# Kernel optimization log

Measured on AMD Instinct MI355X. Metric: run time of the kernel, lower is better.

Reference implementation:

```python
import jax, jax.numpy as jnp
import numpy as np

D_MODEL = 1024
N_HEADS = 16
POINT_DIM = 4
PLUCKER_DIM = 6
PAIRS4 = [(0, 1), (0, 2), (0, 3), (1, 2), (1, 3), (2, 3)]
_J6 = jnp.array([[0, 0, 0, 0, 0, 1], [0, 0, 0, 0, -1, 0], [0, 0, 0, 1, 0, 0],
                 [0, 0, 1, 0, 0, 0], [0, -1, 0, 0, 0, 0], [1, 0, 0, 0, 0, 0]], dtype=jnp.float32)


def exterior(p1, p2):
    # p1, p2: [..., point_dim] -> normalized Plucker coords [..., 6]
    L = jnp.stack([p1[..., i] * p2[..., j] - p1[..., j] * p2[..., i] for i, j in PAIRS4], axis=-1)
    n = jnp.linalg.norm(L, axis=-1, keepdims=True)
    return L / jnp.maximum(n, 1e-12)


def setup_inputs() -> dict:
    key = jax.random.key(0)
    ks = jax.random.split(key, 16)
    B, T, D, H, pd = 2, 1024, D_MODEL, N_HEADS, POINT_DIM
    s = 0.02
    return {
        "x": jax.random.normal(ks[0], (B, T, D), dtype=jnp.float32),
        "qkv_w": jax.random.normal(ks[1], (D, 3 * D), dtype=jnp.float32) * s,
        "qkv_b": jnp.zeros((3 * D,), dtype=jnp.float32),
        "w1_write_w": jax.random.normal(ks[2], (2 * D, pd * H), dtype=jnp.float32) * s,
        "w2_write_w": jax.random.normal(ks[3], (D, pd * H), dtype=jnp.float32) * s,
        "w1_read_w": jax.random.normal(ks[4], (D, pd * H), dtype=jnp.float32) * s,
        "w2_read_w": jax.random.normal(ks[5], (D, pd * H), dtype=jnp.float32) * s,
        "mem_value_w": jax.random.normal(ks[6], (D, D), dtype=jnp.float32) * s,
        "mem_value_b": jnp.zeros((D,), dtype=jnp.float32),
        "mem_gate_w": jax.random.normal(ks[7], (D, H), dtype=jnp.float32) * s,
        "mem_gate_b": jnp.zeros((H,), dtype=jnp.float32),
        "mem_scale": jnp.full((H,), 0.1, dtype=jnp.float32),
        "out_w": jax.random.normal(ks[8], (D, D), dtype=jnp.float32) * s,
        "out_b": jnp.zeros((D,), dtype=jnp.float32),
        "decay_logits": jnp.full((H,), 4.6, dtype=jnp.float32),
        "J": _J6,
    }


def reference(x, qkv_w, qkv_b, w1_write_w, w2_write_w, w1_read_w, w2_read_w,
              mem_value_w, mem_value_b, mem_gate_w, mem_gate_b, mem_scale,
              out_w, out_b, decay_logits, J):
    B, T, D = x.shape
    H = N_HEADS
    dh = D // H
    pd = POINT_DIM
    scale = dh ** (-0.5)

    # ---- standard causal attention ----
    qkv = (x @ qkv_w + qkv_b).reshape(B, T, 3, H, dh)
    q = jnp.transpose(qkv[:, :, 0], (0, 2, 1, 3))  # [B,H,T,dh]
    k = jnp.transpose(qkv[:, :, 1], (0, 2, 1, 3))
    v = jnp.transpose(qkv[:, :, 2], (0, 2, 1, 3))
    scores = jnp.einsum('bhtd,bhsd->bhts', q, k) * scale
    causal_mask = jnp.triu(jnp.ones((T, T), dtype=bool), k=1)
    scores = jnp.where(causal_mask, -jnp.inf, scores)
    attn = jax.nn.softmax(scores, axis=-1)
    seq_out = jnp.einsum('bhts,bhsd->bthd', attn, v).reshape(B, T, D)

    # ---- trigram write lines ----
    z = jnp.zeros((B, 1, D), dtype=x.dtype)
    x_prev1 = jnp.concatenate([z, x[:, :-1]], axis=1)
    x_prev2 = jnp.concatenate([z, z, x[:, :-2]], axis=1)
    trigram_ctx = jnp.concatenate([x_prev2, x_prev1], axis=-1)  # [B,T,2D]
    w1 = (trigram_ctx @ w1_write_w).reshape(B, T, H, pd)
    w2 = (x @ w2_write_w).reshape(B, T, H, pd)
    write_lines = exterior(w1, w2)  # [B,T,H,6]
    r1 = (x @ w1_read_w).reshape(B, T, H, pd)
    r2 = (x @ w2_read_w).reshape(B, T, H, pd)
    read_lines = exterior(r1, r2)  # [B,T,H,6]

    # ---- Plucker incidence + decay weighting ----
    J_write = jnp.einsum('bshi,ij->bshj', write_lines, J)
    incidence = jnp.einsum('bthi,bshi->bhts', read_lines, J_write)  # [B,H,T,T]
    incidence_sq = incidence ** 2
    positions = jnp.arange(T, dtype=x.dtype)
    diffs = positions[:, None] - positions[None, :]  # [T,T]
    decays = jax.nn.sigmoid(decay_logits)  # [H]
    # strictly-causal (diffs>0) decay weights; masked_fill(triu diag=0, 0) == (diffs>0)
    weights = jnp.where(diffs[None] > 0, decays[:, None, None] ** jnp.maximum(diffs, 0.0)[None], 0.0)
    mem_score = jnp.sum(incidence_sq * weights[None], axis=-1)  # [B,H,T]

    # ---- gated memory value ----
    mem_val = x @ mem_value_w + mem_value_b  # [B,T,D]
    gate = jax.nn.sigmoid(x @ mem_gate_w + mem_gate_b)  # [B,T,H]
    mem_score_t = jnp.transpose(mem_score, (0, 2, 1))  # [B,T,H]
    gated = jax.nn.sigmoid(mem_score_t * mem_scale[None, None, :]) * gate
    gated = jnp.mean(gated, axis=-1, keepdims=True)  # [B,T,1]

    return (seq_out + gated * mem_val) @ out_w + out_b
```

## Files before the change

kernel.cpp:

```cpp
#include <hip/hip_runtime.h>
#include <hip/hip_bf16.h>
#include <stdint.h>


typedef __attribute__((ext_vector_type(8))) __bf16 bf16v8;
typedef __attribute__((ext_vector_type(8))) short  s16x8;
typedef __attribute__((ext_vector_type(4))) float  f32x4;

#define LOG2E 1.4426950408889634f

__device__ __forceinline__ float bf2f(short s) {
  union { uint32_t u; float f; } cv; cv.u = ((uint32_t)(uint16_t)s) << 16; return cv.f;
}
__device__ __forceinline__ short f2bf(float f) {
  union { float f; uint32_t u; } cv; cv.f = f;
  uint32_t r = cv.u + 0x7fffu + ((cv.u >> 16) & 1u);
  return (short)(r >> 16);
}

__device__ __forceinline__ f32x4 mfma_bf16(s16x8 a, s16x8 b, f32x4 c) {
  return __builtin_amdgcn_mfma_f32_16x16x32_bf16(
      __builtin_bit_cast(bf16v8, a), __builtin_bit_cast(bf16v8, b), c, 0, 0, 0);
}

__device__ __forceinline__ void gload_lds16(const void* g, void* l) {
  __builtin_amdgcn_global_load_lds(
      (const __attribute__((address_space(1))) uint32_t*)g,
      (__attribute__((address_space(3))) uint32_t*)l, 16, 0, 0);
}


__global__ __launch_bounds__(256) void k_prep(
    const float* __restrict__ x, const float* __restrict__ qkvw,
    const float* __restrict__ mvw, const float* __restrict__ ow,
    const float* __restrict__ w1w, const float* __restrict__ w2w,
    const float* __restrict__ r1w, const float* __restrict__ r2w,
    const float* __restrict__ gw, const float* __restrict__ qkvb,
    const float* __restrict__ mvb,
    short* __restrict__ xb, short* __restrict__ btall, short* __restrict__ owT,
    float* __restrict__ biasAll) {
  __shared__ float tile[32][33];
  const int bid = blockIdx.x;
  const int tid = threadIdx.x;
  if (bid < 2048) {
    const int i = (bid * 256 + tid) * 4;
    float4 v = *(const float4*)&x[i];
    short4 o;
    o.x = f2bf(v.x); o.y = f2bf(v.y); o.z = f2bf(v.z); o.w = f2bf(v.w);
    *(short4*)&xb[i] = o;
    return;
  }
  if (bid < 7168) {
    const float* W; short* Wt; int N, u;
    if (bid < 5120)      { W = qkvw; Wt = btall;                       N = 3072; u = bid - 2048; }
    else if (bid < 6144) { W = mvw;  Wt = btall + (size_t)3072 * 1024; N = 1024; u = bid - 5120; }
    else                 { W = ow;   Wt = owT;                         N = 1024; u = bid - 6144; }
    const int ntiles = N >> 5;
    const int n0 = (u % ntiles) * 32, k0 = (u / ntiles) * 32;
    const int tx = tid & 31, ty = tid >> 5;
#pragma unroll
    for (int i = 0; i < 4; i++)
      tile[ty + i * 8][tx] = W[(size_t)(k0 + ty + i * 8) * N + n0 + tx];
    __syncthreads();
#pragma unroll
    for (int i = 0; i < 4; i++)
      Wt[(size_t)(n0 + ty + i * 8) * 1024 + k0 + tx] = f2bf(tile[tx][ty + i * 8]);
    return;
  }
  if (bid < 8704) {
    const int idx = (bid - 7168) * 256 + tid;
    const int r = idx >> 10, k = idx & 1023;
    float v = 0.f;
    if (r < 64)       v = w1w[(size_t)k * 64 + r];
    else if (r < 128) v = w1w[(size_t)(1024 + k) * 64 + (r - 64)];
    else if (r < 192) v = w2w[(size_t)k * 64 + (r - 128)];
    else if (r < 256) v = r1w[(size_t)k * 64 + (r - 192)];
    else if (r < 320) v = r2w[(size_t)k * 64 + (r - 256)];
    else if (r < 336) v = gw[(size_t)k * 16 + (r - 320)];
    btall[(size_t)4096 * 1024 + idx] = f2bf(v);
    return;
  }
  {
    const int i = (bid - 8704) * 256 + tid;
    if (i < 4480) {
      float v = 0.f;
      if (i < 3072) v = qkvb[i];
      else if (i < 4096) v = mvb[i - 3072];
      biasAll[i] = v;
    }
  }
}


__global__ __launch_bounds__(256) void k_gemmF(const short* __restrict__ A,
                                               const short* __restrict__ Bt,
                                               short* __restrict__ C,
                                               const float* __restrict__ bias,
                                               float* __restrict__ projf) {
  const int N = 4480, K = 1024;
  __shared__ short As[2][128 * 32];
  __shared__ short Bs[2][128 * 32];
  const int m0 = blockIdx.x * 128, n0 = blockIdx.y * 128;
  const int tid = threadIdx.x;
  const int lane = tid & 63, w = tid >> 6;
  const int wr = (w >> 1) * 64, wc = (w & 1) * 64;
  const int l15 = lane & 15, lg = lane >> 4;
  const int r0e = tid >> 2, c0e = (tid & 3) << 3;
  const int r1e = (tid + 256) >> 2, c1e = ((tid + 256) & 3) << 3;
  f32x4 acc[4][4] = {};

  gload_lds16(A + (size_t)(m0 + r0e) * K + c0e, &As[0][tid * 8]);
  gload_lds16(A + (size_t)(m0 + r1e) * K + c1e, &As[0][(tid + 256) * 8]);
  gload_lds16(Bt + (size_t)(n0 + r0e) * K + c0e, &Bs[0][tid * 8]);
  gload_lds16(Bt + (size_t)(n0 + r1e) * K + c1e, &Bs[0][(tid + 256) * 8]);
  __syncthreads();

  const int nkt = K >> 5;
  for (int kt = 0; kt < nkt; kt++) {
    const int cur = kt & 1;
    if (kt + 1 < nkt) {
      const int k0n = (kt + 1) << 5;
      const int nxt = cur ^ 1;
      gload_lds16(A + (size_t)(m0 + r0e) * K + k0n + c0e, &As[nxt][tid * 8]);
      gload_lds16(A + (size_t)(m0 + r1e) * K + k0n + c1e, &As[nxt][(tid + 256) * 8]);
      gload_lds16(Bt + (size_t)(n0 + r0e) * K + k0n + c0e, &Bs[nxt][tid * 8]);
      gload_lds16(Bt + (size_t)(n0 + r1e) * K + k0n + c1e, &Bs[nxt][(tid + 256) * 8]);
    }
    s16x8 af[4], bfv[4];
#pragma unroll
    for (int i = 0; i < 4; i++) {
      af[i]  = *(const s16x8*)&As[cur][(wr + i * 16 + l15) * 32 + lg * 8];
      bfv[i] = *(const s16x8*)&Bs[cur][(wc + i * 16 + l15) * 32 + lg * 8];
    }
    __builtin_amdgcn_s_setprio(1);
#pragma unroll
    for (int mi = 0; mi < 4; mi++)
#pragma unroll
      for (int ni = 0; ni < 4; ni++)
        acc[mi][ni] = mfma_bf16(af[mi], bfv[ni], acc[mi][ni]);
    __builtin_amdgcn_s_setprio(0);
    __syncthreads();
  }
  const bool isproj = (n0 >= 4096);
#pragma unroll
  for (int mi = 0; mi < 4; mi++)
#pragma unroll
    for (int ni = 0; ni < 4; ni++) {
      const int col = n0 + wc + ni * 16 + l15;
      const float bv = bias[col];
#pragma unroll
      for (int r = 0; r < 4; r++) {
        const int row = m0 + wr + mi * 16 + lg * 4 + r;
        const float v = acc[mi][ni][r] + bv;
        if (isproj) projf[(size_t)row * 384 + (col - 4096)] = v;
        else        C[(size_t)row * 4480 + col] = f2bf(v);
      }
    }
}


template <int BM>
__global__ __launch_bounds__(256) void k_gemm(const short* __restrict__ A,
                                              const short* __restrict__ Bt,
                                              float* __restrict__ C,
                                              const float* __restrict__ bias,
                                              int N, int K) {
  constexpr int MI = BM / 32;
  __shared__ short As[2][BM * 32];
  __shared__ short Bs[2][128 * 32];
  const int m0 = blockIdx.x * BM, n0 = blockIdx.y * 128;
  const int tid = threadIdx.x;
  const int lane = tid & 63, w = tid >> 6;
  const int wr = (w >> 1) * (BM / 2), wc = (w & 1) * 64;
  const int l15 = lane & 15, lg = lane >> 4;
  const int r0e = tid >> 2, c0e = (tid & 3) << 3;
  const int r1e = (tid + 256) >> 2, c1e = ((tid + 256) & 3) << 3;
  f32x4 acc[MI][4] = {};

  auto stage = [&](int buf, int k0) {
    if constexpr (BM == 128) {
      gload_lds16(A + (size_t)(m0 + r0e) * K + k0 + c0e, &As[buf][tid * 8]);
      gload_lds16(A + (size_t)(m0 + r1e) * K + k0 + c1e, &As[buf][(tid + 256) * 8]);
    } else {
      gload_lds16(A + (size_t)(m0 + r0e) * K + k0 + c0e, &As[buf][tid * 8]);
    }
    gload_lds16(Bt + (size_t)(n0 + r0e) * K + k0 + c0e, &Bs[buf][tid * 8]);
    gload_lds16(Bt + (size_t)(n0 + r1e) * K + k0 + c1e, &Bs[buf][(tid + 256) * 8]);
  };

  stage(0, 0);
  __syncthreads();
  const int nkt = K >> 5;
  for (int kt = 0; kt < nkt; kt++) {
    const int cur = kt & 1;
    if (kt + 1 < nkt) stage(cur ^ 1, (kt + 1) << 5);
    s16x8 af[MI], bfv[4];
#pragma unroll
    for (int i = 0; i < MI; i++)
      af[i] = *(const s16x8*)&As[cur][(wr + i * 16 + l15) * 32 + lg * 8];
#pragma unroll
    for (int i = 0; i < 4; i++)
      bfv[i] = *(const s16x8*)&Bs[cur][(wc + i * 16 + l15) * 32 + lg * 8];
    __builtin_amdgcn_s_setprio(1);
#pragma unroll
    for (int mi = 0; mi < MI; mi++)
#pragma unroll
      for (int ni = 0; ni < 4; ni++)
        acc[mi][ni] = mfma_bf16(af[mi], bfv[ni], acc[mi][ni]);
    __builtin_amdgcn_s_setprio(0);
    __syncthreads();
  }
#pragma unroll
  for (int mi = 0; mi < MI; mi++)
#pragma unroll
    for (int ni = 0; ni < 4; ni++) {
      const int col = n0 + wc + ni * 16 + l15;
      const float bv = bias ? bias[col] : 0.f;
#pragma unroll
      for (int r = 0; r < 4; r++) {
        const int row = m0 + wr + mi * 16 + lg * 4 + r;
        C[(size_t)row * N + col] = acc[mi][ni][r] + bv;
      }
    }
}


__global__ void k_vtr(const short* __restrict__ fused, short* __restrict__ vtg) {
  __shared__ short tile[32][33];
  const int bh = blockIdx.z;
  const int b = bh >> 4, h = bh & 15;
  const int t0 = blockIdx.x * 32, d0 = blockIdx.y * 32;
  const int tx = threadIdx.x, ty = threadIdx.y;
#pragma unroll
  for (int i = 0; i < 4; i++)
    tile[ty + i * 8][tx] =
        fused[(size_t)(b * 1024 + t0 + ty + i * 8) * 4480 + 2048 + h * 64 + d0 + tx];
  __syncthreads();
#pragma unroll
  for (int i = 0; i < 4; i++)
    vtg[(size_t)(bh * 64 + d0 + ty + i * 8) * 1024 + t0 + tx] = tile[tx][ty + i * 8];
}


__global__ __launch_bounds__(256) void k_attn(const short* __restrict__ fused,
                                              const short* __restrict__ vtg,
                                              float* __restrict__ Of,
                                              float* __restrict__ Ml) {
  const int id = blockIdx.x;
  const int j = 15 - (id >> 6);
  const int rem = id & 63;
  const int sid = rem >> 5, bh = rem & 31;
  const int b = bh >> 4, h = bh & 15;
  const int tid = threadIdx.x, lane = tid & 63, w = tid >> 6;
  const int l15 = lane & 15, lg = lane >> 4;
  const int q0 = j * 64;
  const int nkv = j + 1;
  const int half = (nkv + 1) >> 1;
  const int lo = sid ? half : 0;
  const int hi = sid ? nkv : half;
  const int pidx = ((j * 32 + bh) << 1) | sid;

  __shared__ short Kl[64 * 72];
  __shared__ short Vt[64 * 72];
  __shared__ short Pl[4][16 * 72];
  const short* base = fused + (size_t)b * 1024 * 4480;
  const short* vbase = vtg + (size_t)bh * 64 * 1024;

  const int e0 = tid, e1 = tid + 256;
  const int r0e = e0 >> 3, c0e = (e0 & 7) << 3;
  const int r1e = e1 >> 3, c1e = (e1 & 7) << 3;

  s16x8 qf[2];
#pragma unroll
  for (int ks = 0; ks < 2; ks++)
    qf[ks] = *(const s16x8*)&base[(size_t)(q0 + w * 16 + l15) * 4480 +
                                  h * 64 + ks * 32 + lg * 8];

  f32x4 O[4] = {};
  float m_run[4], l_run[4];
#pragma unroll
  for (int r = 0; r < 4; r++) { m_run[r] = -1e30f; l_run[r] = 0.f; }

  if (lo < hi) {
    const int kv0 = lo * 64;
    s16x8 ka = *(const s16x8*)&base[(size_t)(kv0 + r0e) * 4480 + 1024 + h * 64 + c0e];
    s16x8 kb = *(const s16x8*)&base[(size_t)(kv0 + r1e) * 4480 + 1024 + h * 64 + c1e];
    s16x8 va = *(const s16x8*)&vbase[(size_t)r0e * 1024 + kv0 + c0e];
    s16x8 vb = *(const s16x8*)&vbase[(size_t)r1e * 1024 + kv0 + c1e];
    *(s16x8*)&Kl[r0e * 72 + c0e] = ka;
    *(s16x8*)&Kl[r1e * 72 + c1e] = kb;
    *(s16x8*)&Vt[r0e * 72 + c0e] = va;
    *(s16x8*)&Vt[r1e * 72 + c1e] = vb;
  }
  __syncthreads();

  for (int kt = lo; kt < hi; kt++) {
    const int kv0 = kt * 64;
    const bool pf = (kt + 1 < hi);
    s16x8 kn0, kn1, vn0, vn1;
    if (pf) {
      const int kvn = kv0 + 64;
      kn0 = *(const s16x8*)&base[(size_t)(kvn + r0e) * 4480 + 1024 + h * 64 + c0e];
      kn1 = *(const s16x8*)&base[(size_t)(kvn + r1e) * 4480 + 1024 + h * 64 + c1e];
      vn0 = *(const s16x8*)&vbase[(size_t)r0e * 1024 + kvn + c0e];
      vn1 = *(const s16x8*)&vbase[(size_t)r1e * 1024 + kvn + c1e];
    }

    f32x4 S[4] = {};
    __builtin_amdgcn_s_setprio(1);
#pragma unroll
    for (int sf = 0; sf < 4; sf++) {
      s16x8 kf0 = *(const s16x8*)&Kl[(sf * 16 + l15) * 72 + lg * 8];
      s16x8 kf1 = *(const s16x8*)&Kl[(sf * 16 + l15) * 72 + 32 + lg * 8];
      S[sf] = mfma_bf16(qf[0], kf0, S[sf]);
      S[sf] = mfma_bf16(qf[1], kf1, S[sf]);
    }
    __builtin_amdgcn_s_setprio(0);

    const bool diag = (kt == j);
    float sv[4][4];
#pragma unroll
    for (int sf = 0; sf < 4; sf++)
#pragma unroll
      for (int r = 0; r < 4; r++) {
        float vv = S[sf][r] * 0.125f;
        if (diag) {
          const int sg = kv0 + sf * 16 + l15;
          const int qg = q0 + w * 16 + lg * 4 + r;
          if (sg > qg) vv = -1e30f;
        }
        sv[sf][r] = vv;
      }
#pragma unroll
    for (int r = 0; r < 4; r++) {
      float pm = fmaxf(fmaxf(sv[0][r], sv[1][r]), fmaxf(sv[2][r], sv[3][r]));
      pm = fmaxf(pm, __shfl_xor(pm, 1, 64));
      pm = fmaxf(pm, __shfl_xor(pm, 2, 64));
      pm = fmaxf(pm, __shfl_xor(pm, 4, 64));
      pm = fmaxf(pm, __shfl_xor(pm, 8, 64));
      if (pm > m_run[r] + 8.f) {
        const float fac = exp2f((m_run[r] - pm) * LOG2E);
        m_run[r] = pm;
        l_run[r] *= fac;
#pragma unroll
        for (int nf = 0; nf < 4; nf++) O[nf][r] *= fac;
      }
      float rs = 0.f;
#pragma unroll
      for (int sf = 0; sf < 4; sf++) {
        float p = (sv[sf][r] <= -1e29f) ? 0.f : exp2f((sv[sf][r] - m_run[r]) * LOG2E);
        rs += p;
        Pl[w][(lg * 4 + r) * 72 + sf * 16 + l15] = f2bf(p);
      }
      rs += __shfl_xor(rs, 1, 64);
      rs += __shfl_xor(rs, 2, 64);
      rs += __shfl_xor(rs, 4, 64);
      rs += __shfl_xor(rs, 8, 64);
      l_run[r] += rs;
    }

    __builtin_amdgcn_s_setprio(1);
#pragma unroll
    for (int ks = 0; ks < 2; ks++) {
      s16x8 pfr = *(const s16x8*)&Pl[w][l15 * 72 + ks * 32 + lg * 8];
#pragma unroll
      for (int nf = 0; nf < 4; nf++) {
        s16x8 vf = *(const s16x8*)&Vt[(nf * 16 + l15) * 72 + ks * 32 + lg * 8];
        O[nf] = mfma_bf16(pfr, vf, O[nf]);
      }
    }
    __builtin_amdgcn_s_setprio(0);

    __syncthreads();
    if (pf) {
      *(s16x8*)&Kl[r0e * 72 + c0e] = kn0;
      *(s16x8*)&Kl[r1e * 72 + c1e] = kn1;
      *(s16x8*)&Vt[r0e * 72 + c0e] = vn0;
      *(s16x8*)&Vt[r1e * 72 + c1e] = vn1;
      __syncthreads();
    }
  }

  float* ob = Of + (size_t)pidx * 4096;
  float* mb = Ml + (size_t)pidx * 128;
#pragma unroll
  for (int r = 0; r < 4; r++) {
    const int rloc = w * 16 + lg * 4 + r;
#pragma unroll
    for (int nf = 0; nf < 4; nf++)
      ob[rloc * 64 + nf * 16 + l15] = O[nf][r];
    if (l15 == 0) {
      mb[rloc] = m_run[r];
      mb[64 + rloc] = l_run[r];
    }
  }
}


__device__ __forceinline__ void exterior6(const float p1[4], const float p2[4], float L[6]) {
  L[0] = p1[0] * p2[1] - p1[1] * p2[0];
  L[1] = p1[0] * p2[2] - p1[2] * p2[0];
  L[2] = p1[0] * p2[3] - p1[3] * p2[0];
  L[3] = p1[1] * p2[2] - p1[2] * p2[1];
  L[4] = p1[1] * p2[3] - p1[3] * p2[1];
  L[5] = p1[2] * p2[3] - p1[3] * p2[2];
  float n = sqrtf(L[0] * L[0] + L[1] * L[1] + L[2] * L[2] +
                  L[3] * L[3] + L[4] * L[4] + L[5] * L[5]);
  float inv = 1.f / fmaxf(n, 1e-12f);
#pragma unroll
  for (int j = 0; j < 6; j++) L[j] *= inv;
}

__global__ void k_lines(const float* __restrict__ proj, const float* __restrict__ Jm,
                        float* __restrict__ jw, float* __restrict__ rl) {
  const int idx = blockIdx.x * 256 + threadIdx.x;
  const int t = idx & 1023, h = (idx >> 10) & 15, b = idx >> 14;
  const int n = b * 1024 + t;
  const int bh = b * 16 + h;
  float p1[4], p2[4], L[6];
#pragma unroll
  for (int p = 0; p < 4; p++) {
    float a  = (t >= 2) ? proj[(size_t)(n - 2) * 384 + h * 4 + p] : 0.f;
    float bb = (t >= 1) ? proj[(size_t)(n - 1) * 384 + 64 + h * 4 + p] : 0.f;
    p1[p] = a + bb;
    p2[p] = proj[(size_t)n * 384 + 128 + h * 4 + p];
  }
  exterior6(p1, p2, L);
  const size_t jo = (size_t)bh * 6144 + t;
#pragma unroll
  for (int j = 0; j < 6; j++) {
    float s = 0.f;
#pragma unroll
    for (int i = 0; i < 6; i++) s += L[i] * Jm[i * 6 + j];
    jw[jo + (size_t)j * 1024] = s;
  }
#pragma unroll
  for (int p = 0; p < 4; p++) {
    p1[p] = proj[(size_t)n * 384 + 192 + h * 4 + p];
    p2[p] = proj[(size_t)n * 384 + 256 + h * 4 + p];
  }
  exterior6(p1, p2, L);
  const size_t ro = ((size_t)bh * 1024 + t) * 6;
#pragma unroll
  for (int j = 0; j < 6; j++) rl[ro + j] = L[j];
}


__global__ __launch_bounds__(256) void k_mscore(const float* __restrict__ jw,
                                                const float* __restrict__ rl,
                                                const float* __restrict__ dlog,
                                                float* __restrict__ ms) {
  const int gtid = blockIdx.x * 256 + threadIdx.x;
  const int wid = gtid >> 6, lane = gtid & 63;
  const int bh = wid >> 10, t = wid & 1023;
  const int h = bh & 15, b = bh >> 4;
  const float d = 1.f / (1.f + expf(-dlog[h]));
  const float l2d = log2f(d);
  const float* jwp = jw + (size_t)bh * 6144;
  const float* rp = rl + ((size_t)bh * 1024 + t) * 6;
  const float r0 = rp[0], r1 = rp[1], r2 = rp[2], r3 = rp[3], r4 = rp[4], r5 = rp[5];
  float wgt = exp2f((float)(t - lane) * l2d);
  const float gw = exp2f(-64.f * l2d);
  float acc = 0.f;
  for (int s = lane; s < t; s += 64) {
    const float dot = r0 * jwp[s] + r1 * jwp[1024 + s] + r2 * jwp[2048 + s] +
                      r3 * jwp[3072 + s] + r4 * jwp[4096 + s] + r5 * jwp[5120 + s];
    acc += wgt * dot * dot;
    wgt *= gw;
  }
  acc += __shfl_xor(acc, 1, 64);
  acc += __shfl_xor(acc, 2, 64);
  acc += __shfl_xor(acc, 4, 64);
  acc += __shfl_xor(acc, 8, 64);
  acc += __shfl_xor(acc, 16, 64);
  acc += __shfl_xor(acc, 32, 64);
  if (lane == 0) ms[((size_t)(b * 1024 + t)) * 16 + h] = acc;
}


__global__ __launch_bounds__(256) void k_combine(const float* __restrict__ Of,
                                                 const float* __restrict__ Ml,
                                                 const short* __restrict__ fused,
                                                 const float* __restrict__ proj,
                                                 const float* __restrict__ ms,
                                                 const float* __restrict__ mem_scale,
                                                 const float* __restrict__ gate_b,
                                                 short* __restrict__ comb) {
  const int n = blockIdx.x;
  const int tid = threadIdx.x;
  __shared__ float gsh;
  if (tid < 16) {
    const float gp = proj[(size_t)n * 384 + 320 + tid] + gate_b[tid];
    const float g = 1.f / (1.f + expf(-gp));
    const float sc = ms[(size_t)n * 16 + tid] * mem_scale[tid];
    const float sg = 1.f / (1.f + expf(-sc));
    float v = sg * g;
    v += __shfl_xor(v, 1, 64);
    v += __shfl_xor(v, 2, 64);
    v += __shfl_xor(v, 4, 64);
    v += __shfl_xor(v, 8, 64);
    if (tid == 0) gsh = v * (1.f / 16.f);
  }
  __syncthreads();
  const float g = gsh;
  const int b = n >> 10, t = n & 1023;
  const int c0 = tid * 4;
  const int h = c0 >> 6, coff = c0 & 63;
  const int bh = b * 16 + h;
  const int p = ((t >> 6) * 32 + bh) << 1;
  const int rloc = t & 63;
  const float m0v = Ml[(size_t)p * 128 + rloc];
  const float l0v = Ml[(size_t)p * 128 + 64 + rloc];
  const float m1v = Ml[(size_t)(p + 1) * 128 + rloc];
  const float l1v = Ml[(size_t)(p + 1) * 128 + 64 + rloc];
  const float M = fmaxf(m0v, m1v);
  const float w0 = exp2f((m0v - M) * LOG2E);
  const float w1 = exp2f((m1v - M) * LOG2E);
  const float inv = 1.f / (w0 * l0v + w1 * l1v);
  f32x4 o0 = *(const f32x4*)&Of[(size_t)p * 4096 + rloc * 64 + coff];
  f32x4 o1 = *(const f32x4*)&Of[(size_t)(p + 1) * 4096 + rloc * 64 + coff];
  short4 mvv = *(const short4*)&fused[(size_t)n * 4480 + 3072 + c0];
  short4 ov;
  ov.x = f2bf((w0 * o0[0] + w1 * o1[0]) * inv + g * bf2f(mvv.x));
  ov.y = f2bf((w0 * o0[1] + w1 * o1[1]) * inv + g * bf2f(mvv.y));
  ov.z = f2bf((w0 * o0[2] + w1 * o1[2]) * inv + g * bf2f(mvv.z));
  ov.w = f2bf((w0 * o0[3] + w1 * o1[3]) * inv + g * bf2f(mvv.w));
  *(short4*)&comb[(size_t)n * 1024 + c0] = ov;
}


extern "C" void kernel_launch(void* const* d_in, const int* in_sizes, int n_in,
                              void* d_out, int out_size, void* d_ws, size_t ws_size,
                              hipStream_t stream) {
  const float* x    = (const float*)d_in[0];
  const float* qkvw = (const float*)d_in[1];
  const float* qkvb = (const float*)d_in[2];
  const float* w1w  = (const float*)d_in[3];
  const float* w2w  = (const float*)d_in[4];
  const float* r1w  = (const float*)d_in[5];
  const float* r2w  = (const float*)d_in[6];
  const float* mvw  = (const float*)d_in[7];
  const float* mvb  = (const float*)d_in[8];
  const float* gw   = (const float*)d_in[9];
  const float* gb   = (const float*)d_in[10];
  const float* msc  = (const float*)d_in[11];
  const float* ow   = (const float*)d_in[12];
  const float* ob   = (const float*)d_in[13];
  const float* dlog = (const float*)d_in[14];
  const float* Jm   = (const float*)d_in[15];
  float* out = (float*)d_out;

  char* wsp = (char*)d_ws;
  auto alloc = [&](size_t bytes) {
    char* p = wsp;
    wsp += (bytes + 255) & ~(size_t)255;
    return p;
  };
  short* xb     = (short*)alloc((size_t)2048 * 1024 * 2);
  short* btall  = (short*)alloc((size_t)4480 * 1024 * 2);
  short* owT    = (short*)alloc((size_t)1024 * 1024 * 2);
  short* fusedC = (short*)alloc((size_t)2048 * 4480 * 2);
  float* projf  = (float*)alloc((size_t)2048 * 384 * 4);
  float* biasA  = (float*)alloc((size_t)4480 * 4);
  short* vtg    = (short*)alloc((size_t)32 * 64 * 1024 * 2);
  short* comb   = (short*)alloc((size_t)2048 * 1024 * 2);
  float* jwb    = (float*)alloc((size_t)32 * 6144 * 4);
  float* rlb    = (float*)alloc((size_t)32768 * 6 * 4);
  float* msb    = (float*)alloc((size_t)2048 * 16 * 4);
  float* Of     = (float*)alloc((size_t)1024 * 4096 * 4);
  float* Mlb    = (float*)alloc((size_t)1024 * 128 * 4);

  k_prep<<<8722, 256, 0, stream>>>(x, qkvw, mvw, ow, w1w, w2w, r1w, r2w, gw,
                                   qkvb, mvb, xb, btall, owT, biasA);

  k_gemmF<<<dim3(16, 35), 256, 0, stream>>>(xb, btall, fusedC, biasA, projf);

  k_vtr<<<dim3(32, 2, 32), dim3(32, 8), 0, stream>>>(fusedC, vtg);
  k_attn<<<1024, 256, 0, stream>>>(fusedC, vtg, Of, Mlb);

  k_lines<<<128, 256, 0, stream>>>(projf, Jm, jwb, rlb);
  k_mscore<<<8192, 256, 0, stream>>>(jwb, rlb, dlog, msb);
  k_combine<<<2048, 256, 0, stream>>>(Of, Mlb, fusedC, projf, msb, msc, gb, comb);

  k_gemm<64><<<dim3(32, 8), 256, 0, stream>>>(comb, owT, out, ob, 1024, 1024);
}
```

Measured before the change: 126.9 us.

## Replace quadratic memory-score loop with prefix scan over outer products

Rewrites the decayed squared-incidence sum as a causal prefix sum of decay-weighted symmetric outer products of the J-transformed write lines (21 terms), contracted with the read line's outer product. The exclusive scan is done with wave shuffles plus a shared-memory pass across waves, fusing line construction and scoring into one kernel with one block per batch-head. This removes the O(T^2) per-head loop, two launches and the intermediate buffers. The risk is numerical: weights scaled by d^-t can grow large for big t when decay is small, though with d≈0.99 this stays finite.

```diff
diff --git a/kernel.cpp b/kernel.cpp
--- a/kernel.cpp
+++ b/kernel.cpp
@@ -411,13 +411,20 @@
   for (int j = 0; j < 6; j++) L[j] *= inv;
 }
 
-__global__ void k_lines(const float* __restrict__ proj, const float* __restrict__ Jm,
-                        float* __restrict__ jw, float* __restrict__ rl) {
-  const int idx = blockIdx.x * 256 + threadIdx.x;
-  const int t = idx & 1023, h = (idx >> 10) & 15, b = idx >> 14;
+
+__global__ __launch_bounds__(1024) void k_mscan(const float* __restrict__ proj,
+                                                const float* __restrict__ Jm,
+                                                const float* __restrict__ dlog,
+                                                float* __restrict__ ms) {
+  const int bh = blockIdx.x;
+  const int b = bh >> 4, h = bh & 15;
+  const int t = threadIdx.x;
+  const int lane = t & 63, wv = t >> 6;
   const int n = b * 1024 + t;
-  const int bh = b * 16 + h;
-  float p1[4], p2[4], L[6];
+  const float d = 1.f / (1.f + expf(-dlog[h]));
+  const float l2d = log2f(d);
+
+  float p1[4], p2[4], L[6], Jw[6], rl[6];
 #pragma unroll
   for (int p = 0; p < 4; p++) {
     float a  = (t >= 2) ? proj[(size_t)(n - 2) * 384 + h * 4 + p] : 0.f;
@@ -426,55 +433,65 @@
     p2[p] = proj[(size_t)n * 384 + 128 + h * 4 + p];
   }
   exterior6(p1, p2, L);
-  const size_t jo = (size_t)bh * 6144 + t;
 #pragma unroll
   for (int j = 0; j < 6; j++) {
     float s = 0.f;
 #pragma unroll
     for (int i = 0; i < 6; i++) s += L[i] * Jm[i * 6 + j];
-    jw[jo + (size_t)j * 1024] = s;
+    Jw[j] = s;
   }
 #pragma unroll
   for (int p = 0; p < 4; p++) {
     p1[p] = proj[(size_t)n * 384 + 192 + h * 4 + p];
     p2[p] = proj[(size_t)n * 384 + 256 + h * 4 + p];
   }
-  exterior6(p1, p2, L);
-  const size_t ro = ((size_t)bh * 1024 + t) * 6;
-#pragma unroll
-  for (int j = 0; j < 6; j++) rl[ro + j] = L[j];
-}
-
-
-__global__ __launch_bounds__(256) void k_mscore(const float* __restrict__ jw,
-                                                const float* __restrict__ rl,
-                                                const float* __restrict__ dlog,
-                                                float* __restrict__ ms) {
-  const int gtid = blockIdx.x * 256 + threadIdx.x;
-  const int wid = gtid >> 6, lane = gtid & 63;
-  const int bh = wid >> 10, t = wid & 1023;
-  const int h = bh & 15, b = bh >> 4;
-  const float d = 1.f / (1.f + expf(-dlog[h]));
-  const float l2d = log2f(d);
-  const float* jwp = jw + (size_t)bh * 6144;
-  const float* rp = rl + ((size_t)bh * 1024 + t) * 6;
-  const float r0 = rp[0], r1 = rp[1], r2 = rp[2], r3 = rp[3], r4 = rp[4], r5 = rp[5];
-  float wgt = exp2f((float)(t - lane) * l2d);
-  const float gw = exp2f(-64.f * l2d);
-  float acc = 0.f;
-  for (int s = lane; s < t; s += 64) {
-    const float dot = r0 * jwp[s] + r1 * jwp[1024 + s] + r2 * jwp[2048 + s] +
-                      r3 * jwp[3072 + s] + r4 * jwp[4096 + s] + r5 * jwp[5120 + s];
-    acc += wgt * dot * dot;
-    wgt *= gw;
-  }
-  acc += __shfl_xor(acc, 1, 64);
-  acc += __shfl_xor(acc, 2, 64);
-  acc += __shfl_xor(acc, 4, 64);
-  acc += __shfl_xor(acc, 8, 64);
-  acc += __shfl_xor(acc, 16, 64);
-  acc += __shfl_xor(acc, 32, 64);
-  if (lane == 0) ms[((size_t)(b * 1024 + t)) * 16 + h] = acc;
+  exterior6(p1, p2, rl);
+
+  const float ws = exp2f(-(float)t * l2d);
+  float c[21], loc[21];
+  {
+    int k = 0;
+#pragma unroll
+    for (int i = 0; i < 6; i++)
+#pragma unroll
+      for (int j = i; j < 6; j++) {
+        loc[k] = ws * Jw[i] * Jw[j];
+        c[k] = loc[k];
+        k++;
+      }
+  }
+#pragma unroll
+  for (int off = 1; off < 64; off <<= 1) {
+#pragma unroll
+    for (int k = 0; k < 21; k++) {
+      float u = __shfl_up(c[k], off, 64);
+      if (lane >= off) c[k] += u;
+    }
+  }
+  __shared__ float wsum[16][21];
+  __shared__ float woff[16][21];
+  if (lane == 63)
+#pragma unroll
+    for (int k = 0; k < 21; k++) wsum[wv][k] = c[k];
+  __syncthreads();
+  if (t < 21) {
+    float run = 0.f;
+    for (int w2 = 0; w2 < 16; w2++) { woff[w2][t] = run; run += wsum[w2][t]; }
+  }
+  __syncthreads();
+  float q = 0.f;
+  {
+    int k = 0;
+#pragma unroll
+    for (int i = 0; i < 6; i++)
+#pragma unroll
+      for (int j = i; j < 6; j++) {
+        const float P = woff[wv][k] + (c[k] - loc[k]);
+        q += (i == j ? 1.f : 2.f) * rl[i] * rl[j] * P;
+        k++;
+      }
+  }
+  ms[(size_t)n * 16 + h] = exp2f((float)t * l2d) * q;
 }
 
 
@@ -564,8 +581,6 @@
   float* biasA  = (float*)alloc((size_t)4480 * 4);
   short* vtg    = (short*)alloc((size_t)32 * 64 * 1024 * 2);
   short* comb   = (short*)alloc((size_t)2048 * 1024 * 2);
-  float* jwb    = (float*)alloc((size_t)32 * 6144 * 4);
-  float* rlb    = (float*)alloc((size_t)32768 * 6 * 4);
   float* msb    = (float*)alloc((size_t)2048 * 16 * 4);
   float* Of     = (float*)alloc((size_t)1024 * 4096 * 4);
   float* Mlb    = (float*)alloc((size_t)1024 * 128 * 4);
@@ -578,8 +593,7 @@
   k_vtr<<<dim3(32, 2, 32), dim3(32, 8), 0, stream>>>(fusedC, vtg);
   k_attn<<<1024, 256, 0, stream>>>(fusedC, vtg, Of, Mlb);
 
-  k_lines<<<128, 256, 0, stream>>>(projf, Jm, jwb, rlb);
-  k_mscore<<<8192, 256, 0, stream>>>(jwb, rlb, dlog, msb);
+  k_mscan<<<32, 1024, 0, stream>>>(projf, Jm, dlog, msb);
   k_combine<<<2048, 256, 0, stream>>>(Of, Mlb, fusedC, projf, msb, msc, gb, comb);
 
   k_gemm<64><<<dim3(32, 8), 256, 0, stream>>>(comb, owT, out, ob, 1024, 1024);
```

After: 117.3 us. 7.6% less time.
